# Kernel optimization log

Measured on AMD Instinct MI355X. Metric: run time of the kernel, lower is better.

Reference implementation:

```python
import jax, jax.numpy as jnp
import numpy as np

H = 256       # hidden_size
LAT = 32      # latent_size
AV = 40       # atom vocab size
NB = 4        # bond types
B = 256       # batch (num molecules)
LSRC = 400    # src graph length per molecule
NT = 38400    # topo predictions
NA = 38400    # atom predictions
NBD = 76800   # bond predictions


def _lin(key, fin, fout):
    k1, k2 = jax.random.split(key)
    s = 1.0 / np.sqrt(fin)
    w = jax.random.uniform(k1, (fout, fin), jnp.float32, -s, s)
    b = jax.random.uniform(k2, (fout,), jnp.float32, -s, s)
    return w, b


def setup_inputs() -> dict:
    key = jax.random.key(0)
    ks = jax.random.split(key, 24)
    d = {}
    d['src_graph_vecs'] = jax.random.normal(ks[0], (B, LSRC, LAT), jnp.float32)
    d['topo_vecs'] = jax.random.normal(ks[1], (NT, 2 * H), jnp.float32)
    d['atom_vecs'] = jax.random.normal(ks[2], (NA, 2 * H), jnp.float32)
    d['bond_vecs'] = jax.random.normal(ks[3], (NBD, 3 * H), jnp.float32)
    d['topo_idx'] = jax.random.randint(ks[4], (NT,), 0, B)
    d['atom_idx'] = jax.random.randint(ks[5], (NA,), 0, B)
    d['bond_idx'] = jax.random.randint(ks[6], (NBD,), 0, B)
    d['topo_labels'] = jax.random.randint(ks[7], (NT,), 0, 2)
    d['atom_labels'] = jax.random.randint(ks[8], (NA,), 0, AV)
    d['bond_labels'] = jax.random.randint(ks[9], (NBD,), 0, NB)
    d['A_topo_w'], d['A_topo_b'] = _lin(ks[10], 2 * H, LAT)
    d['A_atom_w'], d['A_atom_b'] = _lin(ks[11], 2 * H, LAT)
    d['A_bond_w'], d['A_bond_b'] = _lin(ks[12], 3 * H, LAT)
    d['topoNN_w1'], d['topoNN_b1'] = _lin(ks[13], 2 * H + LAT, H)
    d['topoNN_w2'], d['topoNN_b2'] = _lin(ks[14], H, 1)
    d['atomNN_w1'], d['atomNN_b1'] = _lin(ks[15], 2 * H + LAT, H)
    d['atomNN_w2'], d['atomNN_b2'] = _lin(ks[16], H, AV)
    d['bondNN_w1'], d['bondNN_b1'] = _lin(ks[17], 3 * H + LAT, H)
    d['bondNN_w2'], d['bondNN_b2'] = _lin(ks[18], H, NB)
    return d


def _attention(src, idx, q_in, Aw, Ab):
    # src: [B, L, LAT]; irregular gather per prediction row
    src_g = src[idx]                                   # [N, L, LAT]
    q = q_in @ Aw.T + Ab                               # [N, LAT]
    att = jax.nn.softmax(jnp.einsum('nld,nd->nl', src_g, q), axis=1)
    return jnp.einsum('nl,nld->nd', att, src_g)        # [N, LAT]


def _mlp(x, w1, b1, w2, b2):
    return jax.nn.relu(x @ w1.T + b1) @ w2.T + b2


def _ce_sum(logits, labels):
    lp = jax.nn.log_softmax(logits, axis=-1)
    return -jnp.sum(jnp.take_along_axis(lp, labels[:, None], axis=-1))


def reference(src_graph_vecs, topo_vecs, atom_vecs, bond_vecs,
              topo_idx, atom_idx, bond_idx,
              topo_labels, atom_labels, bond_labels,
              A_topo_w, A_topo_b, A_atom_w, A_atom_b, A_bond_w, A_bond_b,
              topoNN_w1, topoNN_b1, topoNN_w2, topoNN_b2,
              atomNN_w1, atomNN_b1, atomNN_w2, atomNN_b2,
              bondNN_w1, bondNN_b1, bondNN_w2, bondNN_b2):
    bsz = src_graph_vecs.shape[0]
    # topo head
    t_cxt = _attention(src_graph_vecs, topo_idx, topo_vecs, A_topo_w, A_topo_b)
    t_scores = _mlp(jnp.concatenate([topo_vecs, t_cxt], -1),
                    topoNN_w1, topoNN_b1, topoNN_w2, topoNN_b2)[:, 0]
    yt = topo_labels.astype(jnp.float32)
    topo_loss = jnp.sum(jax.nn.softplus(t_scores) - yt * t_scores)  # BCEWithLogits sum
    topo_acc = jnp.mean(((t_scores > 0).astype(jnp.int32) == topo_labels).astype(jnp.float32))
    # atom head
    a_cxt = _attention(src_graph_vecs, atom_idx, atom_vecs, A_atom_w, A_atom_b)
    a_scores = _mlp(jnp.concatenate([atom_vecs, a_cxt], -1),
                    atomNN_w1, atomNN_b1, atomNN_w2, atomNN_b2)
    atom_loss = _ce_sum(a_scores, atom_labels)
    atom_acc = jnp.mean((jnp.argmax(a_scores, -1) == atom_labels).astype(jnp.float32))
    # bond head
    b_cxt = _attention(src_graph_vecs, bond_idx, bond_vecs, A_bond_w, A_bond_b)
    b_scores = _mlp(jnp.concatenate([bond_vecs, b_cxt], -1),
                    bondNN_w1, bondNN_b1, bondNN_w2, bondNN_b2)
    bond_loss = _ce_sum(b_scores, bond_labels)
    bond_acc = jnp.mean((jnp.argmax(b_scores, -1) == bond_labels).astype(jnp.float32))
    loss = (topo_loss + atom_loss + bond_loss) / bsz
    return (loss, atom_acc, topo_acc, bond_acc)
```

## Files before the change

kernel.cpp:

```cpp
#include <hip/hip_runtime.h>
#include <math.h>

#define LATD 32
#define AV 40
#define NBOND 4
#define BATCH 256
#define LSRC 400
#define NT 38400
#define NA 38400
#define NBD 76800

typedef unsigned short ushort_t;
typedef short short8 __attribute__((ext_vector_type(8)));
typedef float f32x4 __attribute__((ext_vector_type(4)));
typedef unsigned short ushort4v __attribute__((ext_vector_type(4)));
typedef unsigned short ushort8v __attribute__((ext_vector_type(8)));

__device__ __forceinline__ ushort_t f2bf(float f) {
    union { float f; unsigned u; } v; v.f = f;
    unsigned r = v.u + 0x7fffu + ((v.u >> 16) & 1u);
    return (ushort_t)(r >> 16);
}
__device__ __forceinline__ float bf2f(ushort_t u) {
    union { unsigned u; float f; } v; v.u = ((unsigned)u) << 16;
    return v.f;
}

__global__ void init_kernel(float* acc, int* cnt) {
    int t = threadIdx.x;
    if (t < 8) acc[t] = 0.0f;
    cnt[t] = 0; cnt[t + 256] = 0; cnt[t + 512] = 0;
}

__global__ __launch_bounds__(256) void hist_kernel(const int* __restrict__ idx, int N,
                                                   int* __restrict__ cnt) {
    __shared__ int lc[256];
    int t = threadIdx.x;
    lc[t] = 0;
    __syncthreads();
    for (int i = blockIdx.x * 256 + t; i < N; i += gridDim.x * 256)
        atomicAdd(&lc[idx[i]], 1);
    __syncthreads();
    if (lc[t]) atomicAdd(&cnt[t], lc[t]);
}

__global__ __launch_bounds__(256) void scan_kernel(const int* __restrict__ cnt,
                                                   int* __restrict__ cur,
                                                   int* __restrict__ bstart) {
    __shared__ int s[256];
    int t = threadIdx.x;
    for (int h = 0; h < 3; ++h) {
        int v = cnt[h * 256 + t];
        s[t] = v;
        __syncthreads();
        for (int d = 1; d < 256; d <<= 1) {
            int u = (t >= d) ? s[t - d] : 0;
            __syncthreads();
            s[t] += u;
            __syncthreads();
        }
        cur[h * 256 + t] = s[t] - v;
        bstart[h * 256 + t] = s[t] - v;
        __syncthreads();
    }
}

__global__ __launch_bounds__(256) void scatter_kernel(const int* __restrict__ idx, int N,
                                                      int* __restrict__ cur,
                                                      int* __restrict__ bucket) {
    for (int i = blockIdx.x * 256 + threadIdx.x; i < N; i += gridDim.x * 256) {
        int b = idx[i];
        int p = atomicAdd(&cur[b], 1);
        bucket[p] = i;
    }
}

template<int DIN, int MAXT>
__global__ __launch_bounds__(256) void attn_fused_kernel(
    const float* __restrict__ src,
    const float* __restrict__ X,
    const float* __restrict__ Aw,
    const float* __restrict__ Ab,
    const int* __restrict__ bucket,
    const int* __restrict__ bstart,
    const int* __restrict__ cnt,
    ushort_t* __restrict__ cxtb)
{
    const int m = blockIdx.x / MAXT;
    const int t = blockIdx.x % MAXT;
    const int cm = cnt[m];
    if (t * 32 >= cm) return;

    __shared__ __align__(16) char smem[62336];
    ushort_t* sQ      = (ushort_t*)(smem);
    ushort_t* sSrcRow = (ushort_t*)(smem + 2560);
    ushort_t* sXA     = (ushort_t*)(smem + 2560);
    ushort_t* sW      = (ushort_t*)(smem + 2560 + 4608);
    ushort_t* sP      = (ushort_t*)(smem);
    ushort_t* sSrcT   = (ushort_t*)(smem + 34560);
    float*    sStats  = (float*)(smem + 61696);
    int*      sRows   = (int*)(smem + 62208);

    const int tid = threadIdx.x;
    const int wave = tid >> 6, lane = tid & 63;
    const int l15 = lane & 15, quad = lane >> 4;
    const int mt = wave & 1;
    const int nt = wave >> 1;

    if (tid < 32) {
        int p = t * 32 + tid;
        sRows[tid] = (p < cm) ? bucket[bstart[m] + p] : -1;
    }
    __syncthreads();

    const int srow = tid >> 3;
    const int sko  = (tid & 7) * 8;
    const int g_s  = sRows[srow];

    f32x4 qacc = {0.f, 0.f, 0.f, 0.f};
    for (int k0 = 0; k0 < DIN; k0 += 64) {
        float4 v0 = {0,0,0,0}, v1 = {0,0,0,0};
        if (g_s >= 0) {
            const float* xb = X + (size_t)g_s * DIN + k0 + sko;
            v0 = *(const float4*)xb; v1 = *(const float4*)(xb + 4);
        }
        ushort8v px;
        px[0]=f2bf(v0.x); px[1]=f2bf(v0.y); px[2]=f2bf(v0.z); px[3]=f2bf(v0.w);
        px[4]=f2bf(v1.x); px[5]=f2bf(v1.y); px[6]=f2bf(v1.z); px[7]=f2bf(v1.w);
        *(ushort8v*)&sXA[srow * 72 + sko] = px;
        const float* wb = Aw + (size_t)srow * DIN + k0 + sko;
        float4 w0 = *(const float4*)wb, w1 = *(const float4*)(wb + 4);
        ushort8v pw;
        pw[0]=f2bf(w0.x); pw[1]=f2bf(w0.y); pw[2]=f2bf(w0.z); pw[3]=f2bf(w0.w);
        pw[4]=f2bf(w1.x); pw[5]=f2bf(w1.y); pw[6]=f2bf(w1.z); pw[7]=f2bf(w1.w);
        *(ushort8v*)&sW[srow * 72 + sko] = pw;
        __syncthreads();
        short8 a0 = *(const short8*)&sXA[(mt*16 + l15)*72 + quad*8];
        short8 a1 = *(const short8*)&sXA[(mt*16 + l15)*72 + 32 + quad*8];
        short8 b0 = *(const short8*)&sW[(nt*16 + l15)*72 + quad*8];
        short8 b1 = *(const short8*)&sW[(nt*16 + l15)*72 + 32 + quad*8];
        qacc = __builtin_amdgcn_mfma_f32_16x16x32_bf16(a0, b0, qacc, 0, 0, 0);
        qacc = __builtin_amdgcn_mfma_f32_16x16x32_bf16(a1, b1, qacc, 0, 0, 0);
        __syncthreads();
    }
    {
        float bias = Ab[nt*16 + l15];
#pragma unroll
        for (int r = 0; r < 4; ++r)
            sQ[(mt*16 + quad*4 + r) * 40 + nt*16 + l15] = f2bf(qacc[r] + bias);
    }

    const float4* s4 = (const float4*)(src + (size_t)m * (LSRC * LATD));
    for (int i = tid; i < 3200; i += 256) {
        float4 v = s4[i];
        int l = i >> 3, d4 = (i & 7) * 4;
        ushort4v pk;
        pk[0]=f2bf(v.x); pk[1]=f2bf(v.y); pk[2]=f2bf(v.z); pk[3]=f2bf(v.w);
        *(ushort4v*)&sSrcRow[l * 40 + d4] = pk;
    }
    __syncthreads();
    for (int i = tid; i < 32 * 416; i += 256) {
        int d = i & 31, l = i >> 5;
        sSrcT[d * 424 + l] = (l < 400) ? sSrcRow[l * 40 + d] : (ushort_t)0;
    }
    __syncthreads();

    short8 aq = *(const short8*)&sQ[(mt*16 + l15) * 40 + quad*8];
    f32x4 sc[13];
    const int nch = 13 - nt;
#pragma unroll
    for (int j = 0; j < 13; ++j) {
        if (j >= nch) break;
        int c = nt + 2 * j;
        short8 bv = *(const short8*)&sSrcRow[(c*16 + l15) * 40 + quad*8];
        f32x4 z = {0.f, 0.f, 0.f, 0.f};
        sc[j] = __builtin_amdgcn_mfma_f32_16x16x32_bf16(aq, bv, z, 0, 0, 0);
    }

    float Mr[4], Sr[4];
#pragma unroll
    for (int r = 0; r < 4; ++r) {
        float mx = sc[0][r];
#pragma unroll
        for (int j = 1; j < 13; ++j) if (j < nch) mx = fmaxf(mx, sc[j][r]);
        float s = 0.f;
#pragma unroll
        for (int j = 0; j < 13; ++j) if (j < nch) s += __expf(sc[j][r] - mx);
        Mr[r] = mx; Sr[r] = s;
    }
#pragma unroll
    for (int msk = 1; msk < 16; msk <<= 1) {
#pragma unroll
        for (int r = 0; r < 4; ++r) {
            float mo = __shfl_xor(Mr[r], msk, 64);
            float so = __shfl_xor(Sr[r], msk, 64);
            float mn = fmaxf(Mr[r], mo);
            Sr[r] = Sr[r] * __expf(Mr[r] - mn) + so * __expf(mo - mn);
            Mr[r] = mn;
        }
    }
    if (l15 == 0) {
#pragma unroll
        for (int r = 0; r < 4; ++r) {
            sStats[(wave * 16 + quad * 4 + r) * 2 + 0] = Mr[r];
            sStats[(wave * 16 + quad * 4 + r) * 2 + 1] = Sr[r];
        }
    }
    __syncthreads();
    {
        const int pw = wave ^ 2;
#pragma unroll
        for (int r = 0; r < 4; ++r) {
            float mo = sStats[(pw*16 + quad*4 + r)*2 + 0];
            float so = sStats[(pw*16 + quad*4 + r)*2 + 1];
            float mn = fmaxf(Mr[r], mo);
            float L = Sr[r] * __expf(Mr[r] - mn) + so * __expf(mo - mn);
            Mr[r] = mn; Sr[r] = 1.0f / L;
        }
    }
#pragma unroll
    for (int j = 0; j < 13; ++j) {
        if (j >= nch) break;
        int col = (nt + 2 * j) * 16 + l15;
#pragma unroll
        for (int r = 0; r < 4; ++r) {
            int row = mt*16 + quad*4 + r;
            sP[row * 424 + col] = f2bf(__expf(sc[j][r] - Mr[r]) * Sr[r]);
        }
    }
    for (int i = tid; i < 512; i += 256) {
        int row = i >> 4, col = 400 + (i & 15);
        sP[row * 424 + col] = 0;
    }
    __syncthreads();

    f32x4 oac = {0.f, 0.f, 0.f, 0.f};
#pragma unroll
    for (int k0 = 0; k0 < 416; k0 += 32) {
        short8 ap = *(const short8*)&sP[(mt*16 + l15) * 424 + k0 + quad*8];
        short8 bp = *(const short8*)&sSrcT[(nt*16 + l15) * 424 + k0 + quad*8];
        oac = __builtin_amdgcn_mfma_f32_16x16x32_bf16(ap, bp, oac, 0, 0, 0);
    }
    {
        int col = nt*16 + l15;
#pragma unroll
        for (int r = 0; r < 4; ++r) {
            int rowl = mt*16 + quad*4 + r;
            int g = sRows[rowl];
            if (g >= 0) cxtb[(size_t)g * 32 + col] = f2bf(oac[r]);
        }
    }
}

template<int DIN, int DO>
__global__ __launch_bounds__(256) void mlp_mfma_kernel(
    const float* __restrict__ X,
    const ushort_t* __restrict__ cxtb,
    const float* __restrict__ W1,
    const float* __restrict__ B1,
    const float* __restrict__ W2,
    const float* __restrict__ B2,
    const int* __restrict__ labels,
    float* __restrict__ accum,
    int M)
{
    constexpr int DC = DIN + 32;
    constexpr int KITERS = DC / 32;

    __shared__ ushort_t sAB[10240];
    __shared__ ushort_t HS[64 * 256];
    __shared__ float lg[64 * DO];

    ushort_t* As = sAB;
    ushort_t* Bs = sAB + 2048;

    const int tid = threadIdx.x;
    const int row0 = blockIdx.x * 64;
    const int wave = tid >> 6;
    const int lane = tid & 63;
    const int l15 = lane & 15;
    const int l4 = lane >> 4;

    f32x4 acc[4][4];
#pragma unroll
    for (int mi = 0; mi < 4; ++mi)
#pragma unroll
        for (int ni = 0; ni < 4; ++ni)
            acc[mi][ni] = (f32x4){0.f, 0.f, 0.f, 0.f};

    for (int it = 0; it < KITERS; ++it) {
        const int k0 = it * 32;
#pragma unroll
        for (int half = 0; half < 2; ++half) {
            int f = tid + half * 256;
            int row = f >> 3, k4 = (f & 7) * 4;
            ushort4v pk;
            if (k0 < DIN) {
                float4 v = *(const float4*)(X + (size_t)(row0 + row) * DIN + k0 + k4);
                pk[0] = f2bf(v.x); pk[1] = f2bf(v.y);
                pk[2] = f2bf(v.z); pk[3] = f2bf(v.w);
            } else {
                pk = *(const ushort4v*)(cxtb + (size_t)(row0 + row) * 32 + k4);
            }
            *(ushort4v*)&As[row * 32 + k4] = pk;
        }
#pragma unroll
        for (int i = 0; i < 8; ++i) {
            int f = tid + i * 256;
            int n = f >> 3, k4 = (f & 7) * 4;
            float4 v = *(const float4*)(W1 + (size_t)n * DC + k0 + k4);
            ushort4v pk;
            pk[0] = f2bf(v.x); pk[1] = f2bf(v.y);
            pk[2] = f2bf(v.z); pk[3] = f2bf(v.w);
            *(ushort4v*)&Bs[n * 32 + k4] = pk;
        }
        __syncthreads();

        short8 af[4], bfv[4];
#pragma unroll
        for (int mi = 0; mi < 4; ++mi)
            af[mi] = *(const short8*)&As[(mi * 16 + l15) * 32 + l4 * 8];
#pragma unroll
        for (int ni = 0; ni < 4; ++ni)
            bfv[ni] = *(const short8*)&Bs[(wave * 64 + ni * 16 + l15) * 32 + l4 * 8];
#pragma unroll
        for (int mi = 0; mi < 4; ++mi)
#pragma unroll
            for (int ni = 0; ni < 4; ++ni)
                acc[mi][ni] = __builtin_amdgcn_mfma_f32_16x16x32_bf16(
                    af[mi], bfv[ni], acc[mi][ni], 0, 0, 0);
        __syncthreads();
    }

    float b1v[4];
#pragma unroll
    for (int ni = 0; ni < 4; ++ni) b1v[ni] = B1[wave * 64 + ni * 16 + l15];
#pragma unroll
    for (int mi = 0; mi < 4; ++mi) {
#pragma unroll
        for (int ni = 0; ni < 4; ++ni) {
            int col = wave * 64 + ni * 16 + l15;
#pragma unroll
            for (int r = 0; r < 4; ++r) {
                int rowl = mi * 16 + l4 * 4 + r;
                float h = fmaxf(acc[mi][ni][r] + b1v[ni], 0.0f);
                HS[rowl * 256 + col] = f2bf(h);
            }
        }
    }
#pragma unroll 4
    for (int j = 0; j < DO; ++j)
        sAB[j * 256 + tid] = f2bf(W2[(size_t)j * 256 + tid]);
    __syncthreads();

    for (int p = tid; p < 64 * DO; p += 256) {
        int r = p / DO, o = p - (p / DO) * DO;
        float s = 0.0f;
#pragma unroll 4
        for (int kk = 0; kk < 32; ++kk) {
            ushort8v hv = *(const ushort8v*)&HS[r * 256 + kk * 8];
            ushort8v wv = *(const ushort8v*)&sAB[o * 256 + kk * 8];
#pragma unroll
            for (int e = 0; e < 8; ++e) s += bf2f(hv[e]) * bf2f(wv[e]);
        }
        lg[p] = s + B2[o];
    }
    __syncthreads();

    float loss_l = 0.0f, cnt_l = 0.0f;
    if (tid < 64) {
        int lab = labels[row0 + tid];
        if (DO == 1) {
            float s = lg[tid];
            loss_l = fmaxf(s, 0.0f) + log1pf(__expf(-fabsf(s))) - (float)lab * s;
            int pred = (s > 0.0f) ? 1 : 0;
            cnt_l = (pred == lab) ? 1.0f : 0.0f;
        } else {
            const float* lr = &lg[tid * DO];
            float mx = lr[0];
            int am = 0;
#pragma unroll
            for (int o = 1; o < DO; ++o) {
                float v = lr[o];
                if (v > mx) { mx = v; am = o; }
            }
            float se = 0.0f;
#pragma unroll
            for (int o = 0; o < DO; ++o) se += __expf(lr[o] - mx);
            loss_l = mx + logf(se) - lr[lab];
            cnt_l = (am == lab) ? 1.0f : 0.0f;
        }
#pragma unroll
        for (int off = 32; off > 0; off >>= 1) {
            loss_l += __shfl_down(loss_l, off, 64);
            cnt_l  += __shfl_down(cnt_l, off, 64);
        }
        if (tid == 0) {
            atomicAdd(accum, loss_l);
            atomicAdd(accum + 1, cnt_l);
        }
    }
}

__global__ void finalize_kernel(const float* __restrict__ acc, float* __restrict__ out) {
    if (threadIdx.x == 0) {
        out[0] = (acc[0] + acc[2] + acc[4]) / (float)BATCH;
        out[1] = acc[3] / (float)NA;
        out[2] = acc[1] / (float)NT;
        out[3] = acc[5] / (float)NBD;
    }
}

extern "C" void kernel_launch(void* const* d_in, const int* in_sizes, int n_in,
                              void* d_out, int out_size, void* d_ws, size_t ws_size,
                              hipStream_t stream) {
    const float* src      = (const float*)d_in[0];
    const float* topoX    = (const float*)d_in[1];
    const float* atomX    = (const float*)d_in[2];
    const float* bondX    = (const float*)d_in[3];
    const int*   topo_idx = (const int*)d_in[4];
    const int*   atom_idx = (const int*)d_in[5];
    const int*   bond_idx = (const int*)d_in[6];
    const int*   topo_lab = (const int*)d_in[7];
    const int*   atom_lab = (const int*)d_in[8];
    const int*   bond_lab = (const int*)d_in[9];
    const float* Atw = (const float*)d_in[10]; const float* Atb = (const float*)d_in[11];
    const float* Aaw = (const float*)d_in[12]; const float* Aab = (const float*)d_in[13];
    const float* Abw = (const float*)d_in[14]; const float* Abb = (const float*)d_in[15];
    const float* tW1 = (const float*)d_in[16]; const float* tB1 = (const float*)d_in[17];
    const float* tW2 = (const float*)d_in[18]; const float* tB2 = (const float*)d_in[19];
    const float* aW1 = (const float*)d_in[20]; const float* aB1 = (const float*)d_in[21];
    const float* aW2 = (const float*)d_in[22]; const float* aB2 = (const float*)d_in[23];
    const float* bW1 = (const float*)d_in[24]; const float* bB1 = (const float*)d_in[25];
    const float* bW2 = (const float*)d_in[26]; const float* bB2 = (const float*)d_in[27];
    float* out = (float*)d_out;

    char* ws = (char*)d_ws;
    float* acc    = (float*)ws;
    int*   cnt    = (int*)(ws + 256);
    int*   cur    = (int*)(ws + 3328);
    int*   bstart = (int*)(ws + 6400);
    int*   bkt_t  = (int*)(ws + 9472);
    int*   bkt_a  = bkt_t + NT;
    int*   bkt_b  = bkt_a + NA;
    ushort_t* cxtb = (ushort_t*)(ws + 623872);

    hipLaunchKernelGGL(init_kernel, dim3(1), dim3(256), 0, stream, acc, cnt);

    hipLaunchKernelGGL(hist_kernel, dim3(128), dim3(256), 0, stream, topo_idx, NT, cnt + 0);
    hipLaunchKernelGGL(hist_kernel, dim3(128), dim3(256), 0, stream, atom_idx, NA, cnt + 256);
    hipLaunchKernelGGL(hist_kernel, dim3(128), dim3(256), 0, stream, bond_idx, NBD, cnt + 512);
    hipLaunchKernelGGL(scan_kernel, dim3(1), dim3(256), 0, stream, cnt, cur, bstart);
    hipLaunchKernelGGL(scatter_kernel, dim3(256), dim3(256), 0, stream, topo_idx, NT, cur + 0, bkt_t);
    hipLaunchKernelGGL(scatter_kernel, dim3(256), dim3(256), 0, stream, atom_idx, NA, cur + 256, bkt_a);
    hipLaunchKernelGGL(scatter_kernel, dim3(256), dim3(256), 0, stream, bond_idx, NBD, cur + 512, bkt_b);

    hipLaunchKernelGGL((attn_fused_kernel<512, 12>), dim3(256 * 12), dim3(256), 0, stream,
                       src, topoX, Atw, Atb, bkt_t, bstart + 0, cnt + 0, cxtb);
    hipLaunchKernelGGL((mlp_mfma_kernel<512, 1>), dim3(NT / 64), dim3(256), 0, stream,
                       topoX, cxtb, tW1, tB1, tW2, tB2, topo_lab, acc + 0, NT);

    hipLaunchKernelGGL((attn_fused_kernel<512, 12>), dim3(256 * 12), dim3(256), 0, stream,
                       src, atomX, Aaw, Aab, bkt_a, bstart + 256, cnt + 256, cxtb);
    hipLaunchKernelGGL((mlp_mfma_kernel<512, 40>), dim3(NA / 64), dim3(256), 0, stream,
                       atomX, cxtb, aW1, aB1, aW2, aB2, atom_lab, acc + 2, NA);

    hipLaunchKernelGGL((attn_fused_kernel<768, 20>), dim3(256 * 20), dim3(256), 0, stream,
                       src, bondX, Abw, Abb, bkt_b, bstart + 512, cnt + 512, cxtb);
    hipLaunchKernelGGL((mlp_mfma_kernel<768, 4>), dim3(NBD / 64), dim3(256), 0, stream,
                       bondX, cxtb, bW1, bB1, bW2, bB2, bond_lab, acc + 4, NBD);

    hipLaunchKernelGGL(finalize_kernel, dim3(1), dim3(64), 0, stream, acc, out);
}
```

Before: 1.330 ms.

## Split query projection into dense GEMM and amortize src staging across tiles

Moves the attention query projection into a separate coalesced MFMA GEMM kernel that writes bf16 queries to workspace, instead of a gathered per-tile projection. The attention kernel now stages each molecule's source matrix once, transposed in LDS, and loops over several 32-row prediction tiles, reusing it. This removes repeated global src loads and transposes per tile. In exchange it adds a Q round trip through memory, strided LDS reads to form score operands, and fewer blocks in flight.

```diff
diff --git a/kernel.cpp b/kernel.cpp
--- a/kernel.cpp
+++ b/kernel.cpp
@@ -75,31 +75,90 @@
     }
 }
 
-template<int DIN, int MAXT>
-__global__ __launch_bounds__(256) void attn_fused_kernel(
-    const float* __restrict__ src,
+template<int DIN>
+__global__ __launch_bounds__(256) void qproj_kernel(
     const float* __restrict__ X,
     const float* __restrict__ Aw,
     const float* __restrict__ Ab,
+    ushort_t* __restrict__ Qbf)
+{
+    __shared__ ushort_t As[64 * 72];
+    __shared__ ushort_t Bs[32 * 72];
+    const int tid = threadIdx.x;
+    const int wave = tid >> 6, lane = tid & 63;
+    const int l15 = lane & 15, quad = lane >> 4;
+    const int row0 = blockIdx.x * 64;
+
+    const int ar = tid >> 2;
+    const int ak = (tid & 3) * 8;
+    const int br = tid >> 3;
+    const int bk = (tid & 7) * 8;
+
+    f32x4 acc0 = {0.f,0.f,0.f,0.f}, acc1 = {0.f,0.f,0.f,0.f};
+
+    for (int k0 = 0; k0 < DIN; k0 += 64) {
+        {
+            const float* xb = X + (size_t)(row0 + ar) * DIN + k0 + ak;
+            float4 v0 = *(const float4*)xb,        v1 = *(const float4*)(xb + 4);
+            float4 v2 = *(const float4*)(xb + 32), v3 = *(const float4*)(xb + 36);
+            ushort8v p;
+            p[0]=f2bf(v0.x); p[1]=f2bf(v0.y); p[2]=f2bf(v0.z); p[3]=f2bf(v0.w);
+            p[4]=f2bf(v1.x); p[5]=f2bf(v1.y); p[6]=f2bf(v1.z); p[7]=f2bf(v1.w);
+            *(ushort8v*)&As[ar * 72 + ak] = p;
+            p[0]=f2bf(v2.x); p[1]=f2bf(v2.y); p[2]=f2bf(v2.z); p[3]=f2bf(v2.w);
+            p[4]=f2bf(v3.x); p[5]=f2bf(v3.y); p[6]=f2bf(v3.z); p[7]=f2bf(v3.w);
+            *(ushort8v*)&As[ar * 72 + ak + 32] = p;
+        }
+        {
+            const float* wb = Aw + (size_t)br * DIN + k0 + bk;
+            float4 w0 = *(const float4*)wb, w1 = *(const float4*)(wb + 4);
+            ushort8v p;
+            p[0]=f2bf(w0.x); p[1]=f2bf(w0.y); p[2]=f2bf(w0.z); p[3]=f2bf(w0.w);
+            p[4]=f2bf(w1.x); p[5]=f2bf(w1.y); p[6]=f2bf(w1.z); p[7]=f2bf(w1.w);
+            *(ushort8v*)&Bs[br * 72 + bk] = p;
+        }
+        __syncthreads();
+        short8 a0 = *(const short8*)&As[(wave*16 + l15) * 72 + quad*8];
+        short8 a1 = *(const short8*)&As[(wave*16 + l15) * 72 + 32 + quad*8];
+        short8 b0 = *(const short8*)&Bs[l15 * 72 + quad*8];
+        short8 b1 = *(const short8*)&Bs[l15 * 72 + 32 + quad*8];
+        short8 b2 = *(const short8*)&Bs[(16 + l15) * 72 + quad*8];
+        short8 b3 = *(const short8*)&Bs[(16 + l15) * 72 + 32 + quad*8];
+        acc0 = __builtin_amdgcn_mfma_f32_16x16x32_bf16(a0, b0, acc0, 0, 0, 0);
+        acc0 = __builtin_amdgcn_mfma_f32_16x16x32_bf16(a1, b1, acc0, 0, 0, 0);
+        acc1 = __builtin_amdgcn_mfma_f32_16x16x32_bf16(a0, b2, acc1, 0, 0, 0);
+        acc1 = __builtin_amdgcn_mfma_f32_16x16x32_bf16(a1, b3, acc1, 0, 0, 0);
+        __syncthreads();
+    }
+    const float ab0 = Ab[l15];
+    const float ab1 = Ab[16 + l15];
+#pragma unroll
+    for (int r = 0; r < 4; ++r) {
+        int row = row0 + wave*16 + quad*4 + r;
+        Qbf[(size_t)row * 32 + l15]      = f2bf(acc0[r] + ab0);
+        Qbf[(size_t)row * 32 + 16 + l15] = f2bf(acc1[r] + ab1);
+    }
+}
+
+template<int TPB, int NBLK>
+__global__ __launch_bounds__(256) void attn2_kernel(
+    const float* __restrict__ src,
+    const ushort_t* __restrict__ Qbf,
     const int* __restrict__ bucket,
     const int* __restrict__ bstart,
     const int* __restrict__ cnt,
     ushort_t* __restrict__ cxtb)
 {
-    const int m = blockIdx.x / MAXT;
-    const int t = blockIdx.x % MAXT;
+    const int m  = blockIdx.x / NBLK;
+    const int t0 = (blockIdx.x % NBLK) * TPB;
     const int cm = cnt[m];
-    if (t * 32 >= cm) return;
-
-    __shared__ __align__(16) char smem[62336];
-    ushort_t* sQ      = (ushort_t*)(smem);
-    ushort_t* sSrcRow = (ushort_t*)(smem + 2560);
-    ushort_t* sXA     = (ushort_t*)(smem + 2560);
-    ushort_t* sW      = (ushort_t*)(smem + 2560 + 4608);
-    ushort_t* sP      = (ushort_t*)(smem);
-    ushort_t* sSrcT   = (ushort_t*)(smem + 34560);
-    float*    sStats  = (float*)(smem + 61696);
-    int*      sRows   = (int*)(smem + 62208);
+    if (t0 * 32 >= cm) return;
+
+    __shared__ __align__(16) char smem[54272];
+    ushort_t* sSrcT  = (ushort_t*)(smem);
+    ushort_t* sP     = (ushort_t*)(smem + 26752);
+    float*    sStats = (float*)(smem + 53632);
+    int*      sRows  = (int*)(smem + 54144);
 
     const int tid = threadIdx.x;
     const int wave = tid >> 6, lane = tid & 63;
@@ -107,148 +166,128 @@
     const int mt = wave & 1;
     const int nt = wave >> 1;
 
-    if (tid < 32) {
-        int p = t * 32 + tid;
-        sRows[tid] = (p < cm) ? bucket[bstart[m] + p] : -1;
+    {
+        const float4* s4 = (const float4*)(src + (size_t)m * (LSRC * LATD));
+        for (int i = tid; i < 3200; i += 256) {
+            float4 v = s4[i];
+            int l = i >> 3, d4 = (i & 7) * 4;
+            sSrcT[(d4 + 0) * 418 + l] = f2bf(v.x);
+            sSrcT[(d4 + 1) * 418 + l] = f2bf(v.y);
+            sSrcT[(d4 + 2) * 418 + l] = f2bf(v.z);
+            sSrcT[(d4 + 3) * 418 + l] = f2bf(v.w);
+        }
+        for (int i = tid; i < 512; i += 256) {
+            int d = i >> 4, l = 400 + (i & 15);
+            sSrcT[d * 418 + l] = 0;
+        }
+        for (int i = tid; i < 512; i += 256) {
+            int row = i >> 4, col = 400 + (i & 15);
+            sP[row * 420 + col] = 0;
+        }
     }
     __syncthreads();
 
-    const int srow = tid >> 3;
-    const int sko  = (tid & 7) * 8;
-    const int g_s  = sRows[srow];
-
-    f32x4 qacc = {0.f, 0.f, 0.f, 0.f};
-    for (int k0 = 0; k0 < DIN; k0 += 64) {
-        float4 v0 = {0,0,0,0}, v1 = {0,0,0,0};
-        if (g_s >= 0) {
-            const float* xb = X + (size_t)g_s * DIN + k0 + sko;
-            v0 = *(const float4*)xb; v1 = *(const float4*)(xb + 4);
-        }
-        ushort8v px;
-        px[0]=f2bf(v0.x); px[1]=f2bf(v0.y); px[2]=f2bf(v0.z); px[3]=f2bf(v0.w);
-        px[4]=f2bf(v1.x); px[5]=f2bf(v1.y); px[6]=f2bf(v1.z); px[7]=f2bf(v1.w);
-        *(ushort8v*)&sXA[srow * 72 + sko] = px;
-        const float* wb = Aw + (size_t)srow * DIN + k0 + sko;
-        float4 w0 = *(const float4*)wb, w1 = *(const float4*)(wb + 4);
-        ushort8v pw;
-        pw[0]=f2bf(w0.x); pw[1]=f2bf(w0.y); pw[2]=f2bf(w0.z); pw[3]=f2bf(w0.w);
-        pw[4]=f2bf(w1.x); pw[5]=f2bf(w1.y); pw[6]=f2bf(w1.z); pw[7]=f2bf(w1.w);
-        *(ushort8v*)&sW[srow * 72 + sko] = pw;
-        __syncthreads();
-        short8 a0 = *(const short8*)&sXA[(mt*16 + l15)*72 + quad*8];
-        short8 a1 = *(const short8*)&sXA[(mt*16 + l15)*72 + 32 + quad*8];
-        short8 b0 = *(const short8*)&sW[(nt*16 + l15)*72 + quad*8];
-        short8 b1 = *(const short8*)&sW[(nt*16 + l15)*72 + 32 + quad*8];
-        qacc = __builtin_amdgcn_mfma_f32_16x16x32_bf16(a0, b0, qacc, 0, 0, 0);
-        qacc = __builtin_amdgcn_mfma_f32_16x16x32_bf16(a1, b1, qacc, 0, 0, 0);
-        __syncthreads();
-    }
-    {
-        float bias = Ab[nt*16 + l15];
-#pragma unroll
-        for (int r = 0; r < 4; ++r)
-            sQ[(mt*16 + quad*4 + r) * 40 + nt*16 + l15] = f2bf(qacc[r] + bias);
-    }
-
-    const float4* s4 = (const float4*)(src + (size_t)m * (LSRC * LATD));
-    for (int i = tid; i < 3200; i += 256) {
-        float4 v = s4[i];
-        int l = i >> 3, d4 = (i & 7) * 4;
-        ushort4v pk;
-        pk[0]=f2bf(v.x); pk[1]=f2bf(v.y); pk[2]=f2bf(v.z); pk[3]=f2bf(v.w);
-        *(ushort4v*)&sSrcRow[l * 40 + d4] = pk;
-    }
-    __syncthreads();
-    for (int i = tid; i < 32 * 416; i += 256) {
-        int d = i & 31, l = i >> 5;
-        sSrcT[d * 424 + l] = (l < 400) ? sSrcRow[l * 40 + d] : (ushort_t)0;
-    }
-    __syncthreads();
-
-    short8 aq = *(const short8*)&sQ[(mt*16 + l15) * 40 + quad*8];
-    f32x4 sc[13];
-    const int nch = 13 - nt;
-#pragma unroll
-    for (int j = 0; j < 13; ++j) {
-        if (j >= nch) break;
-        int c = nt + 2 * j;
-        short8 bv = *(const short8*)&sSrcRow[(c*16 + l15) * 40 + quad*8];
-        f32x4 z = {0.f, 0.f, 0.f, 0.f};
-        sc[j] = __builtin_amdgcn_mfma_f32_16x16x32_bf16(aq, bv, z, 0, 0, 0);
-    }
-
-    float Mr[4], Sr[4];
-#pragma unroll
-    for (int r = 0; r < 4; ++r) {
-        float mx = sc[0][r];
-#pragma unroll
-        for (int j = 1; j < 13; ++j) if (j < nch) mx = fmaxf(mx, sc[j][r]);
-        float s = 0.f;
-#pragma unroll
-        for (int j = 0; j < 13; ++j) if (j < nch) s += __expf(sc[j][r] - mx);
-        Mr[r] = mx; Sr[r] = s;
-    }
-#pragma unroll
-    for (int msk = 1; msk < 16; msk <<= 1) {
+    const int Tm = (cm + 31) >> 5;
+    const int rem = Tm - t0;
+    const int ntiles = rem < TPB ? rem : TPB;
+
+    for (int tt = 0; tt < ntiles; ++tt) {
+        const int t = t0 + tt;
+        if (tid < 32) {
+            int p = t * 32 + tid;
+            sRows[tid] = (p < cm) ? bucket[bstart[m] + p] : -1;
+        }
+        __syncthreads();
+
+        const int grow = sRows[mt * 16 + l15];
+        short8 aq = {0,0,0,0,0,0,0,0};
+        if (grow >= 0)
+            aq = *(const short8*)(Qbf + (size_t)grow * 32 + quad * 8);
+
+        f32x4 sc[13];
+        const int nch = 13 - nt;
+#pragma unroll
+        for (int j = 0; j < 13; ++j) {
+            if (j >= nch) break;
+            int c = nt + 2 * j;
+            int bbase = quad * 8 * 418 + c * 16 + l15;
+            short8 bv;
+#pragma unroll
+            for (int e = 0; e < 8; ++e) bv[e] = (short)sSrcT[bbase + e * 418];
+            f32x4 z = {0.f, 0.f, 0.f, 0.f};
+            sc[j] = __builtin_amdgcn_mfma_f32_16x16x32_bf16(aq, bv, z, 0, 0, 0);
+        }
+
+        float Mr[4], Sr[4];
 #pragma unroll
         for (int r = 0; r < 4; ++r) {
-            float mo = __shfl_xor(Mr[r], msk, 64);
-            float so = __shfl_xor(Sr[r], msk, 64);
-            float mn = fmaxf(Mr[r], mo);
-            Sr[r] = Sr[r] * __expf(Mr[r] - mn) + so * __expf(mo - mn);
-            Mr[r] = mn;
-        }
-    }
-    if (l15 == 0) {
-#pragma unroll
-        for (int r = 0; r < 4; ++r) {
-            sStats[(wave * 16 + quad * 4 + r) * 2 + 0] = Mr[r];
-            sStats[(wave * 16 + quad * 4 + r) * 2 + 1] = Sr[r];
-        }
-    }
-    __syncthreads();
-    {
-        const int pw = wave ^ 2;
-#pragma unroll
-        for (int r = 0; r < 4; ++r) {
-            float mo = sStats[(pw*16 + quad*4 + r)*2 + 0];
-            float so = sStats[(pw*16 + quad*4 + r)*2 + 1];
-            float mn = fmaxf(Mr[r], mo);
-            float L = Sr[r] * __expf(Mr[r] - mn) + so * __expf(mo - mn);
-            Mr[r] = mn; Sr[r] = 1.0f / L;
-        }
-    }
-#pragma unroll
-    for (int j = 0; j < 13; ++j) {
-        if (j >= nch) break;
-        int col = (nt + 2 * j) * 16 + l15;
-#pragma unroll
-        for (int r = 0; r < 4; ++r) {
-            int row = mt*16 + quad*4 + r;
-            sP[row * 424 + col] = f2bf(__expf(sc[j][r] - Mr[r]) * Sr[r]);
-        }
-    }
-    for (int i = tid; i < 512; i += 256) {
-        int row = i >> 4, col = 400 + (i & 15);
-        sP[row * 424 + col] = 0;
-    }
-    __syncthreads();
-
-    f32x4 oac = {0.f, 0.f, 0.f, 0.f};
-#pragma unroll
-    for (int k0 = 0; k0 < 416; k0 += 32) {
-        short8 ap = *(const short8*)&sP[(mt*16 + l15) * 424 + k0 + quad*8];
-        short8 bp = *(const short8*)&sSrcT[(nt*16 + l15) * 424 + k0 + quad*8];
-        oac = __builtin_amdgcn_mfma_f32_16x16x32_bf16(ap, bp, oac, 0, 0, 0);
-    }
-    {
-        int col = nt*16 + l15;
-#pragma unroll
-        for (int r = 0; r < 4; ++r) {
-            int rowl = mt*16 + quad*4 + r;
-            int g = sRows[rowl];
-            if (g >= 0) cxtb[(size_t)g * 32 + col] = f2bf(oac[r]);
-        }
+            float mx = sc[0][r];
+#pragma unroll
+            for (int j = 1; j < 13; ++j) if (j < nch) mx = fmaxf(mx, sc[j][r]);
+            float s = 0.f;
+#pragma unroll
+            for (int j = 0; j < 13; ++j) if (j < nch) s += __expf(sc[j][r] - mx);
+            Mr[r] = mx; Sr[r] = s;
+        }
+#pragma unroll
+        for (int msk = 1; msk < 16; msk <<= 1) {
+#pragma unroll
+            for (int r = 0; r < 4; ++r) {
+                float mo = __shfl_xor(Mr[r], msk, 64);
+                float so = __shfl_xor(Sr[r], msk, 64);
+                float mn = fmaxf(Mr[r], mo);
+                Sr[r] = Sr[r] * __expf(Mr[r] - mn) + so * __expf(mo - mn);
+                Mr[r] = mn;
+            }
+        }
+        if (l15 == 0) {
+#pragma unroll
+            for (int r = 0; r < 4; ++r) {
+                sStats[(wave * 16 + quad * 4 + r) * 2 + 0] = Mr[r];
+                sStats[(wave * 16 + quad * 4 + r) * 2 + 1] = Sr[r];
+            }
+        }
+        __syncthreads();
+        {
+            const int pw = wave ^ 2;
+#pragma unroll
+            for (int r = 0; r < 4; ++r) {
+                float mo = sStats[(pw * 16 + quad * 4 + r) * 2 + 0];
+                float so = sStats[(pw * 16 + quad * 4 + r) * 2 + 1];
+                float mn = fmaxf(Mr[r], mo);
+                float L = Sr[r] * __expf(Mr[r] - mn) + so * __expf(mo - mn);
+                Mr[r] = mn; Sr[r] = 1.0f / L;
+            }
+        }
+#pragma unroll
+        for (int j = 0; j < 13; ++j) {
+            if (j >= nch) break;
+            int col = (nt + 2 * j) * 16 + l15;
+#pragma unroll
+            for (int r = 0; r < 4; ++r) {
+                int row = mt * 16 + quad * 4 + r;
+                sP[row * 420 + col] = f2bf(__expf(sc[j][r] - Mr[r]) * Sr[r]);
+            }
+        }
+        __syncthreads();
+
+        f32x4 oac = {0.f, 0.f, 0.f, 0.f};
+#pragma unroll
+        for (int k0 = 0; k0 < 416; k0 += 32) {
+            short8 ap = *(const short8*)&sP[(mt * 16 + l15) * 420 + k0 + quad * 8];
+            short8 bp = *(const short8*)&sSrcT[(nt * 16 + l15) * 418 + k0 + quad * 8];
+            oac = __builtin_amdgcn_mfma_f32_16x16x32_bf16(ap, bp, oac, 0, 0, 0);
+        }
+        {
+            int col = nt * 16 + l15;
+#pragma unroll
+            for (int r = 0; r < 4; ++r) {
+                int rowl = mt * 16 + quad * 4 + r;
+                int g = sRows[rowl];
+                if (g >= 0) cxtb[(size_t)g * 32 + col] = f2bf(oac[r]);
+            }
+        }
+        __syncthreads();
     }
 }
 
@@ -444,6 +483,7 @@
     int*   bkt_a  = bkt_t + NT;
     int*   bkt_b  = bkt_a + NA;
     ushort_t* cxtb = (ushort_t*)(ws + 623872);
+    ushort_t* Qbf  = (ushort_t*)(ws + 5539072);
 
     hipLaunchKernelGGL(init_kernel, dim3(1), dim3(256), 0, stream, acc, cnt);
 
@@ -455,18 +495,24 @@
     hipLaunchKernelGGL(scatter_kernel, dim3(256), dim3(256), 0, stream, atom_idx, NA, cur + 256, bkt_a);
     hipLaunchKernelGGL(scatter_kernel, dim3(256), dim3(256), 0, stream, bond_idx, NBD, cur + 512, bkt_b);
 
-    hipLaunchKernelGGL((attn_fused_kernel<512, 12>), dim3(256 * 12), dim3(256), 0, stream,
-                       src, topoX, Atw, Atb, bkt_t, bstart + 0, cnt + 0, cxtb);
+    hipLaunchKernelGGL((qproj_kernel<512>), dim3(NT / 64), dim3(256), 0, stream,
+                       topoX, Atw, Atb, Qbf);
+    hipLaunchKernelGGL((attn2_kernel<4, 3>), dim3(256 * 3), dim3(256), 0, stream,
+                       src, Qbf, bkt_t, bstart + 0, cnt + 0, cxtb);
     hipLaunchKernelGGL((mlp_mfma_kernel<512, 1>), dim3(NT / 64), dim3(256), 0, stream,
                        topoX, cxtb, tW1, tB1, tW2, tB2, topo_lab, acc + 0, NT);
 
-    hipLaunchKernelGGL((attn_fused_kernel<512, 12>), dim3(256 * 12), dim3(256), 0, stream,
-                       src, atomX, Aaw, Aab, bkt_a, bstart + 256, cnt + 256, cxtb);
+    hipLaunchKernelGGL((qproj_kernel<512>), dim3(NA / 64), dim3(256), 0, stream,
+                       atomX, Aaw, Aab, Qbf);
+    hipLaunchKernelGGL((attn2_kernel<4, 3>), dim3(256 * 3), dim3(256), 0, stream,
+                       src, Qbf, bkt_a, bstart + 256, cnt + 256, cxtb);
     hipLaunchKernelGGL((mlp_mfma_kernel<512, 40>), dim3(NA / 64), dim3(256), 0, stream,
                        atomX, cxtb, aW1, aB1, aW2, aB2, atom_lab, acc + 2, NA);
 
-    hipLaunchKernelGGL((attn_fused_kernel<768, 20>), dim3(256 * 20), dim3(256), 0, stream,
-                       src, bondX, Abw, Abb, bkt_b, bstart + 512, cnt + 512, cxtb);
+    hipLaunchKernelGGL((qproj_kernel<768>), dim3(NBD / 64), dim3(256), 0, stream,
+                       bondX, Abw, Abb, Qbf);
+    hipLaunchKernelGGL((attn2_kernel<5, 4>), dim3(256 * 4), dim3(256), 0, stream,
+                       src, Qbf, bkt_b, bstart + 512, cnt + 512, cxtb);
     hipLaunchKernelGGL((mlp_mfma_kernel<768, 4>), dim3(NBD / 64), dim3(256), 0, stream,
                        bondX, cxtb, bW1, bB1, bW2, bB2, bond_lab, acc + 4, NBD);
 
```

New measurement: 1.309 ms. Within noise of the previous version (-1.5%).
